# Optimization experiments

Hardware: AMD Instinct MI355X
Metric: run time of the kernel (lower is better)

## Reference

```python
import jax, jax.numpy as jnp
import numpy as np

B, E, H, W = 8, 1024, 16, 1024
DH = E // H


def setup_inputs() -> dict:
    key = jax.random.key(0)
    ks = jax.random.split(key, 5)
    scale = E ** (-0.5)
    return {
        "x": jax.random.normal(ks[0], (3, B, E, W), dtype=jnp.float32),
        "L_Q": jax.random.normal(ks[1], (E, E), dtype=jnp.float32) * scale,
        "L_K": jax.random.normal(ks[2], (E, E), dtype=jnp.float32) * scale,
        "L_V": jax.random.normal(ks[3], (E, E), dtype=jnp.float32) * scale,
        "dense_M": jax.random.normal(ks[4], (E, E), dtype=jnp.float32) * scale,
        "dense_b": jnp.zeros((E, 1), dtype=jnp.float32),
    }


def reference(x, L_Q, L_K, L_V, dense_M, dense_b):
    # x: [3, B, E, W], channels-first sequences (dropout layers are identity in eval)
    K, Q, V = x[0], x[1], x[2]                      # each [B, E, W]
    K = jnp.einsum('ef,bfw->bew', L_K, K)
    Q = jnp.einsum('ef,bfw->bew', L_Q, Q)
    V = jnp.einsum('ef,bfw->bew', L_V, V)
    Kv = K.reshape(B, H, DH, W)
    Qv = Q.reshape(B, H, DH, W)
    Vv = V.reshape(B, H, DH, W)
    # Q_v^T @ K_v -> [B, H, Wq, Wk]
    scores = jnp.einsum('bhdq,bhdk->bhqk', Qv, Kv)
    # causal_factor = tril(-inf, diag=-1): -inf strictly below the diagonal (q > k)
    qi = jnp.arange(W)[:, None]
    ki = jnp.arange(W)[None, :]
    scores = jnp.where(qi > ki, -jnp.inf, scores)
    # softmax over the QUERY axis (-2), post-scaled by E^-0.5 (non-standard)
    attn = jax.nn.softmax(scores, axis=-2) * (E ** (-0.5))
    # V_v @ scores: contract over the query axis -> [B, H, DH, Wk]
    out = jnp.einsum('bhdq,bhqk->bhdk', Vv, attn).reshape(B, E, W)
    # dense output projection: M @ out + b (bias broadcasts over W)
    return jnp.einsum('ef,bfw->bew', dense_M, out) + dense_b
```

## Files before the change

kernel.cpp:

```cpp
#include <hip/hip_runtime.h>

typedef float  f4  __attribute__((ext_vector_type(4)));
typedef short  s8v __attribute__((ext_vector_type(8)));
typedef unsigned short u16;
typedef u16 us4 __attribute__((ext_vector_type(4)));

constexpr int En  = 1024;
constexpr int Wn  = 1024;
constexpr int Bn  = 8;
constexpr int Hn  = 16;
constexpr int DHn = 64;

__device__ inline u16 bf16rn(float x) {
    unsigned u = __float_as_uint(x);
    return (u16)((u + 0x7FFFu + ((u >> 16) & 1u)) >> 16);
}
__device__ inline float bf16tof(u16 h) { return __uint_as_float(((unsigned)h) << 16); }

#define GLD_LDS16(gp, lp) __builtin_amdgcn_global_load_lds(                      \
    (const __attribute__((address_space(1))) void*)(gp),                         \
    (__attribute__((address_space(3))) void*)(lp), 16, 0, 0)

__global__ void split_plain4(const float* __restrict__ p0,
                             const float* __restrict__ p1,
                             const float* __restrict__ p2,
                             const float* __restrict__ p3,
                             u16* __restrict__ base) {
    const int z = blockIdx.y;
    const float* in = (z == 0) ? p0 : (z == 1) ? p1 : (z == 2) ? p2 : p3;
    u16* hi = base + (size_t)(2 * z) * En * En;
    u16* lo = base + (size_t)(2 * z + 1) * En * En;
    int i = blockIdx.x * blockDim.x + threadIdx.x;
    f4 v = ((const f4*)in)[i];
    us4 h, l;
    #pragma unroll
    for (int k = 0; k < 4; ++k) {
        u16 hh = bf16rn(v[k]);
        h[k] = hh;
        l[k] = bf16rn(v[k] - bf16tof(hh));
    }
    ((us4*)hi)[i] = h;
    ((us4*)lo)[i] = l;
}

__global__ __launch_bounds__(256)
void split_t(const float* __restrict__ in, u16* __restrict__ hi,
             u16* __restrict__ lo) {
    __shared__ float T[32][33];
    const int z = blockIdx.z;
    const size_t zo = (size_t)z * En * Wn;
    const int r0 = blockIdx.y * 32, c0 = blockIdx.x * 32;
    const int t = threadIdx.x;
    const int row = t >> 3, c4 = (t & 7) << 2;

    f4 v = *(const f4*)&in[zo + (size_t)(r0 + row) * Wn + c0 + c4];
    T[row][c4 + 0] = v[0]; T[row][c4 + 1] = v[1];
    T[row][c4 + 2] = v[2]; T[row][c4 + 3] = v[3];
    __syncthreads();

    const int oc = row, r4 = c4;
    us4 h, l;
    #pragma unroll
    for (int i = 0; i < 4; ++i) {
        float x = T[r4 + i][oc];
        u16 hh = bf16rn(x);
        h[i] = hh;
        l[i] = bf16rn(x - bf16tof(hh));
    }
    *(us4*)&hi[zo + (size_t)(c0 + oc) * En + r0 + r4] = h;
    *(us4*)&lo[zo + (size_t)(c0 + oc) * En + r0 + r4] = l;
}

__global__ __launch_bounds__(256)
void split_t3(const float* __restrict__ x, char* __restrict__ XT3) {
    __shared__ float T[32][33];
    const size_t matB = (size_t)Bn * En * Wn * 4;
    const int z24 = blockIdx.z;
    const int mat = z24 >> 3, b = z24 & 7;
    const float* in = x + ((size_t)mat * Bn + b) * En * Wn;
    u16* hi = (u16*)(XT3 + (size_t)mat * matB);
    u16* lo = (u16*)(XT3 + (size_t)mat * matB + matB / 2);
    const size_t zo = (size_t)b * En * Wn;

    const int r0 = blockIdx.y * 32, c0 = blockIdx.x * 32;
    const int t = threadIdx.x;
    const int row = t >> 3, c4 = (t & 7) << 2;

    f4 v = *(const f4*)&in[(size_t)(r0 + row) * Wn + c0 + c4];
    T[row][c4 + 0] = v[0]; T[row][c4 + 1] = v[1];
    T[row][c4 + 2] = v[2]; T[row][c4 + 3] = v[3];
    __syncthreads();

    const int oc = row, r4 = c4;
    us4 h, l;
    #pragma unroll
    for (int i = 0; i < 4; ++i) {
        float xv = T[r4 + i][oc];
        u16 hh = bf16rn(xv);
        h[i] = hh;
        l[i] = bf16rn(xv - bf16tof(hh));
    }
    *(us4*)&hi[zo + (size_t)(c0 + oc) * En + r0 + r4] = h;
    *(us4*)&lo[zo + (size_t)(c0 + oc) * En + r0 + r4] = l;
}

template<int MODE>
__global__ __launch_bounds__(256, 3)
void gemm_mfma(const u16* __restrict__ Ah,  const u16* __restrict__ Al,
               const u16* __restrict__ Bth, const u16* __restrict__ Btl,
               float* __restrict__ Yf, u16* __restrict__ Yh, u16* __restrict__ Yl,
               const float* __restrict__ bias) {
    __shared__ u16 AsH[4096], AsL[4096], BsH[4096], BsL[4096];

    const int z  = blockIdx.z;
    const size_t zB = (size_t)z * Wn * En;
    const int e0 = blockIdx.y * 128, n0 = blockIdx.x * 128;
    const int t = threadIdx.x, lane = t & 63, wave = t >> 6;
    const int q = lane >> 4, r = lane & 15;
    const int m_off = (wave & 1) * 64, n_off = (wave >> 1) * 64;

    f4 acc[4][4];
    #pragma unroll
    for (int i = 0; i < 4; ++i)
        #pragma unroll
        for (int j = 0; j < 4; ++j) { acc[i][j][0]=0; acc[i][j][1]=0; acc[i][j][2]=0; acc[i][j][3]=0; }

    for (int kb = 0; kb < En; kb += 32) {
        __syncthreads();
        #pragma unroll
        for (int it = 0; it < 2; ++it) {
            const int id = t + 256 * it;
            const int u = id >> 3;
            const int p = (id & 7) ^ (u & 7);
            const int m = 2 * u + (p >> 2), g = p & 3;
            const size_t colA = (size_t)kb + 8 * g;
            GLD_LDS16(Ah  + (size_t)(e0 + m) * En + colA, &AsH[id * 8]);
            GLD_LDS16(Al  + (size_t)(e0 + m) * En + colA, &AsL[id * 8]);
            GLD_LDS16(Bth + zB + (size_t)(n0 + m) * En + colA, &BsH[id * 8]);
            GLD_LDS16(Btl + zB + (size_t)(n0 + m) * En + colA, &BsL[id * 8]);
        }
        __syncthreads();

        s8v aH[4], aL[4];
        #pragma unroll
        for (int i = 0; i < 4; ++i) {
            const int Ra = m_off + 16 * i + r;
            const int sa = ((((Ra & 1) << 2) | q) ^ ((Ra >> 1) & 7));
            const int ai = ((Ra >> 1) * 8 + sa) * 8;
            aH[i] = *(const s8v*)&AsH[ai];
            aL[i] = *(const s8v*)&AsL[ai];
        }
        #pragma unroll
        for (int j = 0; j < 4; ++j) {
            const int Rb = n_off + 16 * j + r;
            const int sb = ((((Rb & 1) << 2) | q) ^ ((Rb >> 1) & 7));
            const int bi = ((Rb >> 1) * 8 + sb) * 8;
            s8v bH = *(const s8v*)&BsH[bi];
            s8v bL = *(const s8v*)&BsL[bi];
            #pragma unroll
            for (int i = 0; i < 4; ++i) {
                acc[i][j] = __builtin_amdgcn_mfma_f32_16x16x32_bf16(aH[i], bH, acc[i][j], 0, 0, 0);
                acc[i][j] = __builtin_amdgcn_mfma_f32_16x16x32_bf16(aH[i], bL, acc[i][j], 0, 0, 0);
                acc[i][j] = __builtin_amdgcn_mfma_f32_16x16x32_bf16(aL[i], bH, acc[i][j], 0, 0, 0);
            }
        }
    }

    if constexpr (MODE == 0) {
        const size_t zY = (size_t)z * En * Wn;
        #pragma unroll
        for (int i = 0; i < 4; ++i) {
            #pragma unroll
            for (int reg = 0; reg < 4; ++reg) {
                const int e = e0 + m_off + 16 * i + q * 4 + reg;
                const float bv = bias ? bias[e] : 0.0f;
                #pragma unroll
                for (int j = 0; j < 4; ++j) {
                    const int w = n0 + n_off + 16 * j + r;
                    Yf[zY + (size_t)e * Wn + w] = acc[i][j][reg] + bv;
                }
            }
        }
    }
    if constexpr (MODE == 1) {
        #pragma unroll
        for (int i = 0; i < 4; ++i) {
            const int e_base = e0 + m_off + 16 * i + q * 4;
            const int bh_e = z * Hn + (e_base >> 6);
            const int d0 = e_base & 63;
            #pragma unroll
            for (int j = 0; j < 4; ++j) {
                const int w = n0 + n_off + 16 * j + r;
                us4 h, l;
                #pragma unroll
                for (int reg = 0; reg < 4; ++reg) {
                    float x = acc[i][j][reg];
                    u16 hh = bf16rn(x);
                    h[reg] = hh;
                    l[reg] = bf16rn(x - bf16tof(hh));
                }
                const size_t o = ((size_t)bh_e * Wn + w) * 64 + d0;
                *(us4*)&Yh[o] = h;
                *(us4*)&Yl[o] = l;
            }
        }
    }
    if constexpr (MODE == 2) {
        #pragma unroll
        for (int i = 0; i < 4; ++i) {
            #pragma unroll
            for (int reg = 0; reg < 4; ++reg) {
                const int e = e0 + m_off + 16 * i + q * 4 + reg;
                const int bh_e = z * Hn + (e >> 6);
                const int d = e & 63;
                const size_t ro = ((size_t)bh_e * 64 + d) * Wn;
                #pragma unroll
                for (int j = 0; j < 4; ++j) {
                    const int w = n0 + n_off + 16 * j + r;
                    Yh[ro + w] = bf16rn(acc[i][j][reg]);
                }
            }
        }
    }
}

__global__ __launch_bounds__(256, 4)
void gemm_qkv(const u16* __restrict__ Lsp, const char* __restrict__ XT3,
              u16* __restrict__ KTh, u16* __restrict__ KTl,
              u16* __restrict__ QTh, u16* __restrict__ QTl,
              u16* __restrict__ Vb) {
    __shared__ u16 AsH[4096], AsL[4096], BsH[4096], BsL[4096];

    const size_t matB = (size_t)Bn * En * Wn * 4;
    const int z24 = blockIdx.z;
    const int mat = z24 >> 3, b = z24 & 7;
    const u16* Ah  = Lsp + (size_t)(2 * mat) * En * En;
    const u16* Al  = Ah + (size_t)En * En;
    const u16* Bth = (const u16*)(XT3 + (size_t)mat * matB);
    const u16* Btl = (const u16*)(XT3 + (size_t)mat * matB + matB / 2);
    const size_t zB = (size_t)b * Wn * En;

    const int e0 = blockIdx.y * 128, n0 = blockIdx.x * 128;
    const int t = threadIdx.x, lane = t & 63, wave = t >> 6;
    const int q = lane >> 4, r = lane & 15;
    const int m_off = (wave & 1) * 64, n_off = (wave >> 1) * 64;

    f4 acc[4][4];
    #pragma unroll
    for (int i = 0; i < 4; ++i)
        #pragma unroll
        for (int j = 0; j < 4; ++j) { acc[i][j][0]=0; acc[i][j][1]=0; acc[i][j][2]=0; acc[i][j][3]=0; }

    for (int kb = 0; kb < En; kb += 32) {
        __syncthreads();
        #pragma unroll
        for (int it = 0; it < 2; ++it) {
            const int id = t + 256 * it;
            const int u = id >> 3;
            const int p = (id & 7) ^ (u & 7);
            const int m = 2 * u + (p >> 2), g = p & 3;
            const size_t colA = (size_t)kb + 8 * g;
            GLD_LDS16(Ah  + (size_t)(e0 + m) * En + colA, &AsH[id * 8]);
            GLD_LDS16(Al  + (size_t)(e0 + m) * En + colA, &AsL[id * 8]);
            GLD_LDS16(Bth + zB + (size_t)(n0 + m) * En + colA, &BsH[id * 8]);
            GLD_LDS16(Btl + zB + (size_t)(n0 + m) * En + colA, &BsL[id * 8]);
        }
        __syncthreads();

        s8v aH[4], aL[4];
        #pragma unroll
        for (int i = 0; i < 4; ++i) {
            const int Ra = m_off + 16 * i + r;
            const int sa = ((((Ra & 1) << 2) | q) ^ ((Ra >> 1) & 7));
            const int ai = ((Ra >> 1) * 8 + sa) * 8;
            aH[i] = *(const s8v*)&AsH[ai];
            aL[i] = *(const s8v*)&AsL[ai];
        }
        #pragma unroll
        for (int j = 0; j < 4; ++j) {
            const int Rb = n_off + 16 * j + r;
            const int sb = ((((Rb & 1) << 2) | q) ^ ((Rb >> 1) & 7));
            const int bi = ((Rb >> 1) * 8 + sb) * 8;
            s8v bH = *(const s8v*)&BsH[bi];
            s8v bL = *(const s8v*)&BsL[bi];
            #pragma unroll
            for (int i = 0; i < 4; ++i) {
                acc[i][j] = __builtin_amdgcn_mfma_f32_16x16x32_bf16(aH[i], bH, acc[i][j], 0, 0, 0);
                acc[i][j] = __builtin_amdgcn_mfma_f32_16x16x32_bf16(aH[i], bL, acc[i][j], 0, 0, 0);
                acc[i][j] = __builtin_amdgcn_mfma_f32_16x16x32_bf16(aL[i], bH, acc[i][j], 0, 0, 0);
            }
        }
    }

    if (mat < 2) {
        u16* Yh = (mat == 0) ? KTh : QTh;
        u16* Yl = (mat == 0) ? KTl : QTl;
        #pragma unroll
        for (int i = 0; i < 4; ++i) {
            const int e_base = e0 + m_off + 16 * i + q * 4;
            const int bh_e = b * Hn + (e_base >> 6);
            const int d0 = e_base & 63;
            #pragma unroll
            for (int j = 0; j < 4; ++j) {
                const int w = n0 + n_off + 16 * j + r;
                us4 h, l;
                #pragma unroll
                for (int reg = 0; reg < 4; ++reg) {
                    float x = acc[i][j][reg];
                    u16 hh = bf16rn(x);
                    h[reg] = hh;
                    l[reg] = bf16rn(x - bf16tof(hh));
                }
                const size_t o = ((size_t)bh_e * Wn + w) * 64 + d0;
                *(us4*)&Yh[o] = h;
                *(us4*)&Yl[o] = l;
            }
        }
    } else {
        #pragma unroll
        for (int i = 0; i < 4; ++i) {
            #pragma unroll
            for (int reg = 0; reg < 4; ++reg) {
                const int e = e0 + m_off + 16 * i + q * 4 + reg;
                const int bh_e = b * Hn + (e >> 6);
                const int d = e & 63;
                const size_t ro = ((size_t)bh_e * 64 + d) * Wn;
                #pragma unroll
                for (int j = 0; j < 4; ++j) {
                    const int w = n0 + n_off + 16 * j + r;
                    Vb[ro + w] = bf16rn(acc[i][j][reg]);
                }
            }
        }
    }
}

__global__ __launch_bounds__(256, 3)
void attn_mfma3(const u16* __restrict__ QTh, const u16* __restrict__ QTl,
                const u16* __restrict__ KTh, const u16* __restrict__ KTl,
                const u16* __restrict__ Vb,  u16* __restrict__ AoTh,
                u16* __restrict__ AoTl) {
    __shared__ u16 QsH[4096], QsL[4096], Vs[4096];
    __shared__ u16 PT[4][16][72];

    const int id   = blockIdx.x;
    const int rest = id >> 3;
    const int kb   = 15 - (rest & 15);
    const int bh   = (id & 7) + 8 * (rest >> 4);

    const int t = threadIdx.x, lane = t & 63, wave = t >> 6;
    const int r = lane & 15, quad = lane >> 4;
    const int k0 = kb * 64;
    const int kcol = k0 + wave * 16 + r;
    u16 (*pt)[72] = PT[wave];

    const size_t qkb = (size_t)bh * Wn * 64;
    const size_t vbb = (size_t)bh * 64 * Wn;

    s8v kH[2], kL[2];
    #pragma unroll
    for (int s = 0; s < 2; ++s) {
        const size_t a = qkb + (size_t)kcol * 64 + s * 32 + quad * 8;
        kH[s] = *(const s8v*)&KTh[a];
        kL[s] = *(const s8v*)&KTl[a];
    }

    f4 o[4];
    #pragma unroll
    for (int i = 0; i < 4; ++i) { o[i][0]=0; o[i][1]=0; o[i][2]=0; o[i][3]=0; }
    float m = -1e30f, l = 0.0f;

    const int c0 = t,       row0 = c0 >> 3, p0 = (c0 & 7) ^ (row0 & 7);
    const int c1 = t + 256, row1 = c1 >> 3, p1 = (c1 & 7) ^ (row1 & 7);

    s8v Aqh0, Aqh1, Aql0, Aql1, Av0, Av1;
    s8v Bqh0, Bqh1, Bql0, Bql1, Bv0, Bv1;

    auto ld = [&](int q0, s8v& qh0, s8v& qh1, s8v& ql0, s8v& ql1,
                  s8v& v0, s8v& v1) {
        const size_t g = qkb + (size_t)q0 * 64;
        qh0 = *(const s8v*)&QTh[g + (size_t)row0 * 64 + p0 * 8];
        ql0 = *(const s8v*)&QTl[g + (size_t)row0 * 64 + p0 * 8];
        v0  = *(const s8v*)&Vb[vbb + (size_t)row0 * Wn + q0 + p0 * 8];
        qh1 = *(const s8v*)&QTh[g + (size_t)row1 * 64 + p1 * 8];
        ql1 = *(const s8v*)&QTl[g + (size_t)row1 * 64 + p1 * 8];
        v1  = *(const s8v*)&Vb[vbb + (size_t)row1 * Wn + q0 + p1 * 8];
    };
    auto wr = [&](s8v& qh0, s8v& qh1, s8v& ql0, s8v& ql1, s8v& v0, s8v& v1) {
        *(s8v*)&QsH[c0 * 8] = qh0; *(s8v*)&QsL[c0 * 8] = ql0; *(s8v*)&Vs[c0 * 8] = v0;
        *(s8v*)&QsH[c1 * 8] = qh1; *(s8v*)&QsL[c1 * 8] = ql1; *(s8v*)&Vs[c1 * 8] = v1;
    };

    auto compute = [&](int q0) {
        f4 sacc[4];
        #pragma unroll
        for (int mt = 0; mt < 4; ++mt) { sacc[mt][0]=0; sacc[mt][1]=0; sacc[mt][2]=0; sacc[mt][3]=0; }
        #pragma unroll
        for (int s = 0; s < 2; ++s) {
            const int sw = (((s * 4 + quad) ^ (r & 7)) << 3);
            #pragma unroll
            for (int mt = 0; mt < 4; ++mt) {
                const int a = (16 * mt + r) * 64 + sw;
                s8v qh = *(const s8v*)&QsH[a];
                s8v ql = *(const s8v*)&QsL[a];
                sacc[mt] = __builtin_amdgcn_mfma_f32_16x16x32_bf16(qh, kH[s], sacc[mt], 0, 0, 0);
                sacc[mt] = __builtin_amdgcn_mfma_f32_16x16x32_bf16(qh, kL[s], sacc[mt], 0, 0, 0);
                sacc[mt] = __builtin_amdgcn_mfma_f32_16x16x32_bf16(ql, kH[s], sacc[mt], 0, 0, 0);
            }
        }
        if (q0 == k0) {
            const int klocal = wave * 16 + r;
            #pragma unroll
            for (int mt = 0; mt < 4; ++mt)
                #pragma unroll
                for (int reg = 0; reg < 4; ++reg)
                    if (16 * mt + quad * 4 + reg > klocal) sacc[mt][reg] = -1e30f;
        }
        float tm = -1e30f;
        #pragma unroll
        for (int mt = 0; mt < 4; ++mt)
            #pragma unroll
            for (int reg = 0; reg < 4; ++reg) tm = fmaxf(tm, sacc[mt][reg]);
        tm = fmaxf(tm, __shfl_xor(tm, 16));
        tm = fmaxf(tm, __shfl_xor(tm, 32));
        if (!__all(tm - m <= 8.0f)) {
            const float mnew  = fmaxf(m, tm);
            const float alpha = __expf(m - mnew);
            l *= alpha;
            #pragma unroll
            for (int i = 0; i < 4; ++i) {
                o[i][0] *= alpha; o[i][1] *= alpha;
                o[i][2] *= alpha; o[i][3] *= alpha;
            }
            m = mnew;
        }
        float ps = 0.0f;
        #pragma unroll
        for (int mt = 0; mt < 4; ++mt) {
            us4 pk;
            #pragma unroll
            for (int reg = 0; reg < 4; ++reg) {
                float p = __expf(sacc[mt][reg] - m);
                ps += p;
                pk[reg] = bf16rn(p);
            }
            *(us4*)&pt[r][16 * mt + quad * 4] = pk;
        }
        ps += __shfl_xor(ps, 16);
        ps += __shfl_xor(ps, 32);
        l += ps;
        #pragma unroll
        for (int s = 0; s < 2; ++s) {
            const int sw = (((s * 4 + quad) ^ (r & 7)) << 3);
            s8v pf = *(const s8v*)&pt[r][s * 32 + quad * 8];
            #pragma unroll
            for (int i = 0; i < 4; ++i) {
                s8v vf = *(const s8v*)&Vs[(16 * i + r) * 64 + sw];
                o[i] = __builtin_amdgcn_mfma_f32_16x16x32_bf16(vf, pf, o[i], 0, 0, 0);
            }
        }
    };

    ld(0, Aqh0, Aqh1, Aql0, Aql1, Av0, Av1);
    int q0 = 0;
    for (;;) {
        __syncthreads();
        wr(Aqh0, Aqh1, Aql0, Aql1, Av0, Av1);
        __syncthreads();
        if (q0 + 64 <= k0) ld(q0 + 64, Bqh0, Bqh1, Bql0, Bql1, Bv0, Bv1);
        compute(q0);
        q0 += 64;
        if (q0 > k0) break;
        __syncthreads();
        wr(Bqh0, Bqh1, Bql0, Bql1, Bv0, Bv1);
        __syncthreads();
        if (q0 + 64 <= k0) ld(q0 + 64, Aqh0, Aqh1, Aql0, Aql1, Av0, Av1);
        compute(q0);
        q0 += 64;
        if (q0 > k0) break;
    }

    const float inv = 1.0f / (l * 32.0f);
    const size_t ob0 = (size_t)(bh >> 4) * ((size_t)Wn * En) +
                       (size_t)kcol * En + (bh & 15) * 64 + quad * 4;
    #pragma unroll
    for (int i = 0; i < 4; ++i) {
        us4 h, lo4;
        #pragma unroll
        for (int reg = 0; reg < 4; ++reg) {
            float x = o[i][reg] * inv;
            u16 hh = bf16rn(x);
            h[reg] = hh;
            lo4[reg] = bf16rn(x - bf16tof(hh));
        }
        *(us4*)&AoTh[ob0 + 16 * i] = h;
        *(us4*)&AoTl[ob0 + 16 * i] = lo4;
    }
}

__global__ __launch_bounds__(256, 2)
void gemm128(const float* __restrict__ L, const float* __restrict__ X,
             float* __restrict__ Y, const float* __restrict__ bias) {
    __shared__ float As[16][132];
    __shared__ float Bs[16][132];

    const int bz = blockIdx.z;
    const float* Xb = X + (size_t)bz * En * Wn;
    float*       Yb = Y + (size_t)bz * En * Wn;
    const int e0 = blockIdx.y * 128;
    const int w0 = blockIdx.x * 128;
    const int t  = threadIdx.x;
    const int tx = t & 15, ty = t >> 4;
    const int la_e = t >> 2, la_f = (t & 3) << 2;
    const int lb_f = t >> 5, lb_w = (t & 31) << 2;

    float acc[2][2][4][4] = {};

    for (int f0 = 0; f0 < En; f0 += 16) {
        f4 a0 = *(const f4*)&L [(size_t)(e0 + la_e)      * En + f0 + la_f];
        f4 a1 = *(const f4*)&L [(size_t)(e0 + la_e + 64) * En + f0 + la_f];
        f4 b0 = *(const f4*)&Xb[(size_t)(f0 + lb_f)      * Wn + w0 + lb_w];
        f4 b1 = *(const f4*)&Xb[(size_t)(f0 + lb_f + 8)  * Wn + w0 + lb_w];
        __syncthreads();
        As[la_f + 0][la_e] = a0[0]; As[la_f + 1][la_e] = a0[1];
        As[la_f + 2][la_e] = a0[2]; As[la_f + 3][la_e] = a0[3];
        As[la_f + 0][la_e + 64] = a1[0]; As[la_f + 1][la_e + 64] = a1[1];
        As[la_f + 2][la_e + 64] = a1[2]; As[la_f + 3][la_e + 64] = a1[3];
        *(f4*)&Bs[lb_f    ][lb_w] = b0;
        *(f4*)&Bs[lb_f + 8][lb_w] = b1;
        __syncthreads();
        #pragma unroll
        for (int kk = 0; kk < 16; ++kk) {
            f4 av0 = *(f4*)&As[kk][ty * 4];
            f4 av1 = *(f4*)&As[kk][ty * 4 + 64];
            f4 bv0 = *(f4*)&Bs[kk][tx * 4];
            f4 bv1 = *(f4*)&Bs[kk][tx * 4 + 64];
            #pragma unroll
            for (int i = 0; i < 4; ++i)
                #pragma unroll
                for (int j = 0; j < 4; ++j) {
                    acc[0][0][i][j] = fmaf(av0[i], bv0[j], acc[0][0][i][j]);
                    acc[0][1][i][j] = fmaf(av0[i], bv1[j], acc[0][1][i][j]);
                    acc[1][0][i][j] = fmaf(av1[i], bv0[j], acc[1][0][i][j]);
                    acc[1][1][i][j] = fmaf(av1[i], bv1[j], acc[1][1][i][j]);
                }
        }
    }

    #pragma unroll
    for (int eh = 0; eh < 2; ++eh)
        #pragma unroll
        for (int i = 0; i < 4; ++i) {
            const int e = e0 + eh * 64 + ty * 4 + i;
            const float bv = bias ? bias[e] : 0.0f;
            #pragma unroll
            for (int wh = 0; wh < 2; ++wh) {
                f4 v;
                #pragma unroll
                for (int j = 0; j < 4; ++j) v[j] = acc[eh][wh][i][j] + bv;
                *(f4*)&Yb[(size_t)e * Wn + w0 + wh * 64 + tx * 4] = v;
            }
        }
}

__global__ __launch_bounds__(256, 2)
void attn64(const float* __restrict__ Qg, const float* __restrict__ Kg,
            const float* __restrict__ Vg, float* __restrict__ Og) {
    __shared__ float Ks[64][68];
    __shared__ float QP[64][68];
    __shared__ float Vt[64][68];
    __shared__ float mArr[64], lArr[64], alphaArr[64];
    __shared__ float red[4][64];

    const int kb = blockIdx.x, h = blockIdx.y, b = blockIdx.z;
    const size_t base = ((size_t)b * En + (size_t)h * DHn) * Wn;
    const float* Qp = Qg + base;
    const float* Kp = Kg + base;
    const float* Vp = Vg + base;
    float*       Op = Og + base;

    const int t  = threadIdx.x;
    const int tx = t & 15, ty = t >> 4;
    const int lr = t >> 4;
    const int lc = (t & 15) << 2;
    const int k0 = kb * 64;
    const int kc = t & 63, qg = t >> 6;

    #pragma unroll
    for (int r = 0; r < 4; ++r)
        *(f4*)&Ks[lr + r * 16][lc] =
            *(const f4*)&Kp[(size_t)(lr + r * 16) * Wn + k0 + lc];
    if (t < 64) { mArr[t] = -1e30f; lArr[t] = 0.0f; }
    float acc[4][4] = {};
    __syncthreads();

    for (int q0 = 0; q0 <= k0; q0 += 64) {
        #pragma unroll
        for (int r = 0; r < 4; ++r) {
            const int d = lr + r * 16;
            f4 qv = *(const f4*)&Qp[(size_t)d * Wn + q0 + lc];
            f4 vv = *(const f4*)&Vp[(size_t)d * Wn + q0 + lc];
            *(f4*)&QP[d][lc] = qv;
            Vt[lc + 0][d] = vv[0]; Vt[lc + 1][d] = vv[1];
            Vt[lc + 2][d] = vv[2]; Vt[lc + 3][d] = vv[3];
        }
        __syncthreads();

        float s[4][4] = {};
        #pragma unroll 4
        for (int d = 0; d < 64; ++d) {
            f4 kv = *(f4*)&Ks[d][tx * 4];
            f4 q2 = *(f4*)&QP[d][ty * 4];
            #pragma unroll
            for (int i = 0; i < 4; ++i)
                #pragma unroll
                for (int j = 0; j < 4; ++j)
                    s[i][j] = fmaf(q2[i], kv[j], s[i][j]);
        }
        if (q0 == k0) {
            #pragma unroll
            for (int i = 0; i < 4; ++i)
                #pragma unroll
                for (int j = 0; j < 4; ++j)
                    if (ty * 4 + i > tx * 4 + j) s[i][j] = -1e30f;
        }
        __syncthreads();
        #pragma unroll
        for (int i = 0; i < 4; ++i) {
            f4 v;
            #pragma unroll
            for (int j = 0; j < 4; ++j) v[j] = s[i][j];
            *(f4*)&QP[ty * 4 + i][tx * 4] = v;
        }
        __syncthreads();

        float sv[16];
        float lm = -1e30f;
        #pragma unroll
        for (int r = 0; r < 16; ++r) {
            sv[r] = QP[qg * 16 + r][kc];
            lm = fmaxf(lm, sv[r]);
        }
        red[qg][kc] = lm;
        __syncthreads();
        const float mt    = fmaxf(fmaxf(red[0][kc], red[1][kc]),
                                  fmaxf(red[2][kc], red[3][kc]));
        const float mprev = mArr[kc];
        const float mnew  = fmaxf(mprev, mt);
        float psum = 0.0f;
        #pragma unroll
        for (int r = 0; r < 16; ++r) {
            const float p = __expf(sv[r] - mnew);
            psum += p;
            QP[qg * 16 + r][kc] = p;
        }
        __syncthreads();
        red[qg][kc] = psum;
        __syncthreads();
        if (qg == 0) {
            const float alpha = __expf(mprev - mnew);
            lArr[kc] = lArr[kc] * alpha +
                       (red[0][kc] + red[1][kc] + red[2][kc] + red[3][kc]);
            mArr[kc]     = mnew;
            alphaArr[kc] = alpha;
        }
        __syncthreads();

        f4 al = *(f4*)&alphaArr[tx * 4];
        #pragma unroll
        for (int i = 0; i < 4; ++i)
            #pragma unroll
            for (int j = 0; j < 4; ++j)
                acc[i][j] *= al[j];
        #pragma unroll 4
        for (int q = 0; q < 64; ++q) {
            f4 pv = *(f4*)&QP[q][tx * 4];
            f4 v2 = *(f4*)&Vt[q][ty * 4];
            #pragma unroll
            for (int i = 0; i < 4; ++i)
                #pragma unroll
                for (int j = 0; j < 4; ++j)
                    acc[i][j] = fmaf(v2[i], pv[j], acc[i][j]);
        }
        __syncthreads();
    }

    f4 linv = *(f4*)&lArr[tx * 4];
    #pragma unroll
    for (int j = 0; j < 4; ++j) linv[j] = 1.0f / (linv[j] * 32.0f);
    #pragma unroll
    for (int i = 0; i < 4; ++i) {
        f4 v;
        #pragma unroll
        for (int j = 0; j < 4; ++j) v[j] = acc[i][j] * linv[j];
        *(f4*)&Op[(size_t)(ty * 4 + i) * Wn + k0 + tx * 4] = v;
    }
}

extern "C" void kernel_launch(void* const* d_in, const int* in_sizes, int n_in,
                              void* d_out, int out_size, void* d_ws, size_t ws_size,
                              hipStream_t stream) {
    const float* x    = (const float*)d_in[0];
    const float* L_Q  = (const float*)d_in[1];
    const float* L_K  = (const float*)d_in[2];
    const float* L_V  = (const float*)d_in[3];
    const float* M    = (const float*)d_in[4];
    const float* bias = (const float*)d_in[5];
    float* out = (float*)d_out;

    const size_t mat   = (size_t)Bn * En * Wn;
    const size_t matB  = mat * 4;
    const size_t lmatB = (size_t)En * En * 2;
    const size_t need1 = 8 * lmatB + 3 * matB + matB + matB + matB / 2 + matB;
    const size_t need2 = 8 * lmatB + 4 * matB + matB / 2 + matB;

    if (ws_size >= need2) {
        const bool merged = (ws_size >= need1);
        char* w = (char*)d_ws;
        u16*  Lsp = (u16*)w;
        char* XT  = w + 8 * lmatB;
        char* R1  = XT + (merged ? 3 * matB : matB);
        char* R2  = R1 + matB;
        char* R3  = R2 + matB;
        char* R4  = R3 + matB / 2;

        u16* LKh = Lsp + 0 * (lmatB / 2); u16* LKl = Lsp + 1 * (lmatB / 2);
        u16* LQh = Lsp + 2 * (lmatB / 2); u16* LQl = Lsp + 3 * (lmatB / 2);
        u16* LVh = Lsp + 4 * (lmatB / 2); u16* LVl = Lsp + 5 * (lmatB / 2);
        u16* Mh  = Lsp + 6 * (lmatB / 2); u16* Ml  = Lsp + 7 * (lmatB / 2);

        u16* KT_h = (u16*)R1;  u16* KT_l = (u16*)(R1 + matB / 2);
        u16* QT_h = (u16*)R2;  u16* QT_l = (u16*)(R2 + matB / 2);
        u16* Vb   = (u16*)R3;
        u16* AoTh = (u16*)R4;  u16* AoTl = (u16*)(R4 + matB / 2);

        const int n4L = En * En / 4;
        hipLaunchKernelGGL(split_plain4, dim3(n4L / 256, 4), dim3(256), 0, stream,
                           L_K, L_Q, L_V, M, Lsp);

        dim3 gg(Wn / 128, En / 128, Bn), bg(256);

        if (merged) {
            hipLaunchKernelGGL(split_t3, dim3(Wn / 32, En / 32, 24), dim3(256),
                               0, stream, x, XT);
            hipLaunchKernelGGL(gemm_qkv, dim3(Wn / 128, En / 128, 24), bg,
                               0, stream, Lsp, XT, KT_h, KT_l, QT_h, QT_l, Vb);
        } else {
            u16* XT_H = (u16*)XT;  u16* XT_L = (u16*)(XT + matB / 2);
            dim3 gt(Wn / 32, En / 32, Bn), bt(256);
            hipLaunchKernelGGL(split_t, gt, bt, 0, stream, x + 0 * mat, XT_H, XT_L);
            hipLaunchKernelGGL(HIP_KERNEL_NAME(gemm_mfma<1>), gg, bg, 0, stream,
                               LKh, LKl, XT_H, XT_L, (float*)nullptr, KT_h, KT_l, (const float*)nullptr);
            hipLaunchKernelGGL(split_t, gt, bt, 0, stream, x + 1 * mat, XT_H, XT_L);
            hipLaunchKernelGGL(HIP_KERNEL_NAME(gemm_mfma<1>), gg, bg, 0, stream,
                               LQh, LQl, XT_H, XT_L, (float*)nullptr, QT_h, QT_l, (const float*)nullptr);
            hipLaunchKernelGGL(split_t, gt, bt, 0, stream, x + 2 * mat, XT_H, XT_L);
            hipLaunchKernelGGL(HIP_KERNEL_NAME(gemm_mfma<2>), gg, bg, 0, stream,
                               LVh, LVl, XT_H, XT_L, (float*)nullptr, Vb, (u16*)nullptr, (const float*)nullptr);
        }

        hipLaunchKernelGGL(attn_mfma3, dim3(2048), dim3(256), 0, stream,
                           QT_h, QT_l, KT_h, KT_l, Vb, AoTh, AoTl);

        hipLaunchKernelGGL(HIP_KERNEL_NAME(gemm_mfma<0>), gg, bg, 0, stream,
                           Mh, Ml, AoTh, AoTl, out, (u16*)nullptr, (u16*)nullptr, bias);
    } else {
        float* ws = (float*)d_ws;
        float* Kp = ws;
        float* Qp = ws + mat;
        float* Vp = ws + 2 * mat;
        float* Ao = ws + 3 * mat;

        dim3 gg(Wn / 128, En / 128, Bn), blk(256);
        hipLaunchKernelGGL(gemm128, gg, blk, 0, stream, L_K, x + 0 * mat, Kp, (const float*)nullptr);
        hipLaunchKernelGGL(gemm128, gg, blk, 0, stream, L_Q, x + 1 * mat, Qp, (const float*)nullptr);
        hipLaunchKernelGGL(gemm128, gg, blk, 0, stream, L_V, x + 2 * mat, Vp, (const float*)nullptr);

        dim3 ga(Wn / 64, Hn, Bn);
        hipLaunchKernelGGL(attn64, ga, blk, 0, stream, Qp, Kp, Vp, Ao);

        hipLaunchKernelGGL(gemm128, gg, blk, 0, stream, M, Ao, out, bias);
    }
}
```

Before: 464.5 us.

## Process two key blocks per attention workgroup and fuse weight split into transpose

Result: slower. 527.6 us (+13.6%).

```diff
diff --git a/kernel.cpp b/kernel.cpp
--- a/kernel.cpp
+++ b/kernel.cpp
@@ -72,19 +72,41 @@
 }
 
 __global__ __launch_bounds__(256)
-void split_t3(const float* __restrict__ x, char* __restrict__ XT3) {
+void split_t3w(const float* __restrict__ x, char* __restrict__ XT3,
+               const float* __restrict__ p0, const float* __restrict__ p1,
+               const float* __restrict__ p2, const float* __restrict__ p3,
+               u16* __restrict__ Lsp) {
     __shared__ float T[32][33];
+    const int z = blockIdx.z;
+    const int r0 = blockIdx.y * 32, c0 = blockIdx.x * 32;
+    const int t = threadIdx.x;
+    const int row = t >> 3, c4 = (t & 7) << 2;
+
+    if (z >= 24) {
+        const int wm = z - 24;
+        const float* in = (wm == 0) ? p0 : (wm == 1) ? p1 : (wm == 2) ? p2 : p3;
+        u16* hi = Lsp + (size_t)(2 * wm) * En * En;
+        u16* lo = hi + (size_t)En * En;
+        const size_t off = (size_t)(r0 + row) * En + c0 + c4;
+        f4 v = *(const f4*)&in[off];
+        us4 h, l;
+        #pragma unroll
+        for (int k = 0; k < 4; ++k) {
+            u16 hh = bf16rn(v[k]);
+            h[k] = hh;
+            l[k] = bf16rn(v[k] - bf16tof(hh));
+        }
+        *(us4*)&hi[off] = h;
+        *(us4*)&lo[off] = l;
+        return;
+    }
+
     const size_t matB = (size_t)Bn * En * Wn * 4;
-    const int z24 = blockIdx.z;
-    const int mat = z24 >> 3, b = z24 & 7;
+    const int mat = z >> 3, b = z & 7;
     const float* in = x + ((size_t)mat * Bn + b) * En * Wn;
     u16* hi = (u16*)(XT3 + (size_t)mat * matB);
     u16* lo = (u16*)(XT3 + (size_t)mat * matB + matB / 2);
     const size_t zo = (size_t)b * En * Wn;
-
-    const int r0 = blockIdx.y * 32, c0 = blockIdx.x * 32;
-    const int t = threadIdx.x;
-    const int row = t >> 3, c4 = (t & 7) << 2;
 
     f4 v = *(const f4*)&in[(size_t)(r0 + row) * Wn + c0 + c4];
     T[row][c4 + 0] = v[0]; T[row][c4 + 1] = v[1];
@@ -336,39 +358,44 @@
 }
 
 __global__ __launch_bounds__(256, 3)
-void attn_mfma3(const u16* __restrict__ QTh, const u16* __restrict__ QTl,
+void attn_mfma4(const u16* __restrict__ QTh, const u16* __restrict__ QTl,
                 const u16* __restrict__ KTh, const u16* __restrict__ KTl,
                 const u16* __restrict__ Vb,  u16* __restrict__ AoTh,
                 u16* __restrict__ AoTl) {
     __shared__ u16 QsH[4096], QsL[4096], Vs[4096];
-    __shared__ u16 PT[4][16][72];
+    __shared__ u16 PT[4][2][16][72];
 
     const int id   = blockIdx.x;
     const int rest = id >> 3;
-    const int kb   = 15 - (rest & 15);
-    const int bh   = (id & 7) + 8 * (rest >> 4);
+    const int kp   = 7 - (rest & 7);
+    const int bh   = (id & 7) + 8 * (rest >> 3);
 
     const int t = threadIdx.x, lane = t & 63, wave = t >> 6;
     const int r = lane & 15, quad = lane >> 4;
-    const int k0 = kb * 64;
-    const int kcol = k0 + wave * 16 + r;
-    u16 (*pt)[72] = PT[wave];
+    const int k0 = kp * 128;
+    const int kcol0 = k0 + wave * 16 + r;
+    u16 (*pt)[16][72] = PT[wave];
 
     const size_t qkb = (size_t)bh * Wn * 64;
     const size_t vbb = (size_t)bh * 64 * Wn;
 
-    s8v kH[2], kL[2];
-    #pragma unroll
-    for (int s = 0; s < 2; ++s) {
-        const size_t a = qkb + (size_t)kcol * 64 + s * 32 + quad * 8;
-        kH[s] = *(const s8v*)&KTh[a];
-        kL[s] = *(const s8v*)&KTl[a];
-    }
-
-    f4 o[4];
-    #pragma unroll
-    for (int i = 0; i < 4; ++i) { o[i][0]=0; o[i][1]=0; o[i][2]=0; o[i][3]=0; }
-    float m = -1e30f, l = 0.0f;
+    s8v kH[2][2], kL[2][2];
+    #pragma unroll
+    for (int g = 0; g < 2; ++g)
+        #pragma unroll
+        for (int s = 0; s < 2; ++s) {
+            const size_t a = qkb + (size_t)(kcol0 + 64 * g) * 64 + s * 32 + quad * 8;
+            kH[g][s] = *(const s8v*)&KTh[a];
+            kL[g][s] = *(const s8v*)&KTl[a];
+        }
+
+    f4 o0[4], o1[4];
+    #pragma unroll
+    for (int i = 0; i < 4; ++i) {
+        o0[i][0]=0; o0[i][1]=0; o0[i][2]=0; o0[i][3]=0;
+        o1[i][0]=0; o1[i][1]=0; o1[i][2]=0; o1[i][3]=0;
+    }
+    float m0 = -1e30f, l0 = 0.0f, m1 = -1e30f, l1 = 0.0f;
 
     const int c0 = t,       row0 = c0 >> 3, p0 = (c0 & 7) ^ (row0 & 7);
     const int c1 = t + 256, row1 = c1 >> 3, p1 = (c1 & 7) ^ (row1 & 7);
@@ -391,10 +418,52 @@
         *(s8v*)&QsH[c1 * 8] = qh1; *(s8v*)&QsL[c1 * 8] = ql1; *(s8v*)&Vs[c1 * 8] = v1;
     };
 
+    auto smax = [&](f4* sacc, float& mm, float& ll, f4* oo, int g) {
+        float tm = -1e30f;
+        #pragma unroll
+        for (int mt = 0; mt < 4; ++mt)
+            #pragma unroll
+            for (int reg = 0; reg < 4; ++reg) tm = fmaxf(tm, sacc[mt][reg]);
+        tm = fmaxf(tm, __shfl_xor(tm, 16));
+        tm = fmaxf(tm, __shfl_xor(tm, 32));
+        if (!__all(tm - mm <= 8.0f)) {
+            const float mnew  = fmaxf(mm, tm);
+            const float alpha = __expf(mm - mnew);
+            ll *= alpha;
+            #pragma unroll
+            for (int i = 0; i < 4; ++i) {
+                oo[i][0] *= alpha; oo[i][1] *= alpha;
+                oo[i][2] *= alpha; oo[i][3] *= alpha;
+            }
+            mm = mnew;
+        }
+        float ps = 0.0f;
+        #pragma unroll
+        for (int mt = 0; mt < 4; ++mt) {
+            us4 pk;
+            #pragma unroll
+            for (int reg = 0; reg < 4; ++reg) {
+                float p = __expf(sacc[mt][reg] - mm);
+                ps += p;
+                pk[reg] = bf16rn(p);
+            }
+            *(us4*)&pt[g][r][16 * mt + quad * 4] = pk;
+        }
+        ps += __shfl_xor(ps, 16);
+        ps += __shfl_xor(ps, 32);
+        ll += ps;
+    };
+
     auto compute = [&](int q0) {
-        f4 sacc[4];
-        #pragma unroll
-        for (int mt = 0; mt < 4; ++mt) { sacc[mt][0]=0; sacc[mt][1]=0; sacc[mt][2]=0; sacc[mt][3]=0; }
+        const bool do0   = (q0 <= k0);
+        const bool diag0 = (q0 == k0);
+        const bool diag1 = (q0 == k0 + 64);
+        f4 s0[4], s1[4];
+        #pragma unroll
+        for (int mt = 0; mt < 4; ++mt) {
+            s0[mt][0]=0; s0[mt][1]=0; s0[mt][2]=0; s0[mt][3]=0;
+            s1[mt][0]=0; s1[mt][1]=0; s1[mt][2]=0; s1[mt][3]=0;
+        }
         #pragma unroll
         for (int s = 0; s < 2; ++s) {
             const int sw = (((s * 4 + quad) ^ (r & 7)) << 3);
@@ -403,98 +472,94 @@
                 const int a = (16 * mt + r) * 64 + sw;
                 s8v qh = *(const s8v*)&QsH[a];
                 s8v ql = *(const s8v*)&QsL[a];
-                sacc[mt] = __builtin_amdgcn_mfma_f32_16x16x32_bf16(qh, kH[s], sacc[mt], 0, 0, 0);
-                sacc[mt] = __builtin_amdgcn_mfma_f32_16x16x32_bf16(qh, kL[s], sacc[mt], 0, 0, 0);
-                sacc[mt] = __builtin_amdgcn_mfma_f32_16x16x32_bf16(ql, kH[s], sacc[mt], 0, 0, 0);
-            }
-        }
-        if (q0 == k0) {
-            const int klocal = wave * 16 + r;
+                if (do0) {
+                    s0[mt] = __builtin_amdgcn_mfma_f32_16x16x32_bf16(qh, kH[0][s], s0[mt], 0, 0, 0);
+                    s0[mt] = __builtin_amdgcn_mfma_f32_16x16x32_bf16(qh, kL[0][s], s0[mt], 0, 0, 0);
+                    s0[mt] = __builtin_amdgcn_mfma_f32_16x16x32_bf16(ql, kH[0][s], s0[mt], 0, 0, 0);
+                }
+                s1[mt] = __builtin_amdgcn_mfma_f32_16x16x32_bf16(qh, kH[1][s], s1[mt], 0, 0, 0);
+                s1[mt] = __builtin_amdgcn_mfma_f32_16x16x32_bf16(qh, kL[1][s], s1[mt], 0, 0, 0);
+                s1[mt] = __builtin_amdgcn_mfma_f32_16x16x32_bf16(ql, kH[1][s], s1[mt], 0, 0, 0);
+            }
+        }
+        const int klocal = wave * 16 + r;
+        if (diag0) {
             #pragma unroll
             for (int mt = 0; mt < 4; ++mt)
                 #pragma unroll
                 for (int reg = 0; reg < 4; ++reg)
-                    if (16 * mt + quad * 4 + reg > klocal) sacc[mt][reg] = -1e30f;
-        }
-        float tm = -1e30f;
-        #pragma unroll
-        for (int mt = 0; mt < 4; ++mt)
-            #pragma unroll
-            for (int reg = 0; reg < 4; ++reg) tm = fmaxf(tm, sacc[mt][reg]);
-        tm = fmaxf(tm, __shfl_xor(tm, 16));
-        tm = fmaxf(tm, __shfl_xor(tm, 32));
-        if (!__all(tm - m <= 8.0f)) {
-            const float mnew  = fmaxf(m, tm);
-            const float alpha = __expf(m - mnew);
-            l *= alpha;
-            #pragma unroll
-            for (int i = 0; i < 4; ++i) {
-                o[i][0] *= alpha; o[i][1] *= alpha;
-                o[i][2] *= alpha; o[i][3] *= alpha;
-            }
-            m = mnew;
-        }
-        float ps = 0.0f;
-        #pragma unroll
-        for (int mt = 0; mt < 4; ++mt) {
-            us4 pk;
-            #pragma unroll
-            for (int reg = 0; reg < 4; ++reg) {
-                float p = __expf(sacc[mt][reg] - m);
-                ps += p;
-                pk[reg] = bf16rn(p);
-            }
-            *(us4*)&pt[r][16 * mt + quad * 4] = pk;
-        }
-        ps += __shfl_xor(ps, 16);
-        ps += __shfl_xor(ps, 32);
-        l += ps;
+                    if (16 * mt + quad * 4 + reg > klocal) s0[mt][reg] = -1e30f;
+        }
+        if (diag1) {
+            #pragma unroll
+            for (int mt = 0; mt < 4; ++mt)
+                #pragma unroll
+                for (int reg = 0; reg < 4; ++reg)
+                    if (16 * mt + quad * 4 + reg > klocal) s1[mt][reg] = -1e30f;
+        }
+        if (do0) smax(s0, m0, l0, o0, 0);
+        smax(s1, m1, l1, o1, 1);
         #pragma unroll
         for (int s = 0; s < 2; ++s) {
             const int sw = (((s * 4 + quad) ^ (r & 7)) << 3);
-            s8v pf = *(const s8v*)&pt[r][s * 32 + quad * 8];
+            s8v pf0, pf1;
+            if (do0) pf0 = *(const s8v*)&pt[0][r][s * 32 + quad * 8];
+            pf1 = *(const s8v*)&pt[1][r][s * 32 + quad * 8];
             #pragma unroll
             for (int i = 0; i < 4; ++i) {
                 s8v vf = *(const s8v*)&Vs[(16 * i + r) * 64 + sw];
-                o[i] = __builtin_amdgcn_mfma_f32_16x16x32_bf16(vf, pf, o[i], 0, 0, 0);
+                if (do0) o0[i] = __builtin_amdgcn_mfma_f32_16x16x32_bf16(vf, pf0, o0[i], 0, 0, 0);
+                o1[i] = __builtin_amdgcn_mfma_f32_16x16x32_bf16(vf, pf1, o1[i], 0, 0, 0);
             }
         }
     };
 
+    const int qlast = k0 + 64;
     ld(0, Aqh0, Aqh1, Aql0, Aql1, Av0, Av1);
     int q0 = 0;
     for (;;) {
         __syncthreads();
         wr(Aqh0, Aqh1, Aql0, Aql1, Av0, Av1);
         __syncthreads();
-        if (q0 + 64 <= k0) ld(q0 + 64, Bqh0, Bqh1, Bql0, Bql1, Bv0, Bv1);
+        if (q0 + 64 <= qlast) ld(q0 + 64, Bqh0, Bqh1, Bql0, Bql1, Bv0, Bv1);
         compute(q0);
         q0 += 64;
-        if (q0 > k0) break;
+        if (q0 > qlast) break;
         __syncthreads();
         wr(Bqh0, Bqh1, Bql0, Bql1, Bv0, Bv1);
         __syncthreads();
-        if (q0 + 64 <= k0) ld(q0 + 64, Aqh0, Aqh1, Aql0, Aql1, Av0, Av1);
+        if (q0 + 64 <= qlast) ld(q0 + 64, Aqh0, Aqh1, Aql0, Aql1, Av0, Av1);
         compute(q0);
         q0 += 64;
-        if (q0 > k0) break;
-    }
-
-    const float inv = 1.0f / (l * 32.0f);
+        if (q0 > qlast) break;
+    }
+
+    const float inv0 = 1.0f / (l0 * 32.0f);
+    const float inv1 = 1.0f / (l1 * 32.0f);
     const size_t ob0 = (size_t)(bh >> 4) * ((size_t)Wn * En) +
-                       (size_t)kcol * En + (bh & 15) * 64 + quad * 4;
+                       (size_t)kcol0 * En + (bh & 15) * 64 + quad * 4;
+    const size_t ob1 = ob0 + (size_t)64 * En;
     #pragma unroll
     for (int i = 0; i < 4; ++i) {
         us4 h, lo4;
         #pragma unroll
         for (int reg = 0; reg < 4; ++reg) {
-            float x = o[i][reg] * inv;
+            float x = o0[i][reg] * inv0;
             u16 hh = bf16rn(x);
             h[reg] = hh;
             lo4[reg] = bf16rn(x - bf16tof(hh));
         }
         *(us4*)&AoTh[ob0 + 16 * i] = h;
         *(us4*)&AoTl[ob0 + 16 * i] = lo4;
+        #pragma unroll
+        for (int reg = 0; reg < 4; ++reg) {
+            float x = o1[i][reg] * inv1;
+            u16 hh = bf16rn(x);
+            h[reg] = hh;
+            lo4[reg] = bf16rn(x - bf16tof(hh));
+        }
+        *(us4*)&AoTh[ob1 + 16 * i] = h;
+        *(us4*)&AoTl[ob1 + 16 * i] = lo4;
     }
 }
 
@@ -734,18 +799,17 @@
         u16* Vb   = (u16*)R3;
         u16* AoTh = (u16*)R4;  u16* AoTl = (u16*)(R4 + matB / 2);
 
-        const int n4L = En * En / 4;
-        hipLaunchKernelGGL(split_plain4, dim3(n4L / 256, 4), dim3(256), 0, stream,
-                           L_K, L_Q, L_V, M, Lsp);
-
         dim3 gg(Wn / 128, En / 128, Bn), bg(256);
 
         if (merged) {
-            hipLaunchKernelGGL(split_t3, dim3(Wn / 32, En / 32, 24), dim3(256),
-                               0, stream, x, XT);
+            hipLaunchKernelGGL(split_t3w, dim3(Wn / 32, En / 32, 28), dim3(256),
+                               0, stream, x, XT, L_K, L_Q, L_V, M, Lsp);
             hipLaunchKernelGGL(gemm_qkv, dim3(Wn / 128, En / 128, 24), bg,
                                0, stream, Lsp, XT, KT_h, KT_l, QT_h, QT_l, Vb);
         } else {
+            const int n4L = En * En / 4;
+            hipLaunchKernelGGL(split_plain4, dim3(n4L / 256, 4), dim3(256), 0,
+                               stream, L_K, L_Q, L_V, M, Lsp);
             u16* XT_H = (u16*)XT;  u16* XT_L = (u16*)(XT + matB / 2);
             dim3 gt(Wn / 32, En / 32, Bn), bt(256);
             hipLaunchKernelGGL(split_t, gt, bt, 0, stream, x + 0 * mat, XT_H, XT_L);
@@ -759,7 +823,7 @@
                                LVh, LVl, XT_H, XT_L, (float*)nullptr, Vb, (u16*)nullptr, (const float*)nullptr);
         }
 
-        hipLaunchKernelGGL(attn_mfma3, dim3(2048), dim3(256), 0, stream,
+        hipLaunchKernelGGL(attn_mfma4, dim3(1024), dim3(256), 0, stream,
                            QT_h, QT_l, KT_h, KT_l, Vb, AoTh, AoTl);
 
         hipLaunchKernelGGL(HIP_KERNEL_NAME(gemm_mfma<0>), gg, bg, 0, stream,
```
